# Kernel optimization log

Hardware: AMD Instinct MI355X
Metric: run time of the kernel (lower is better)

The kernel has to match this reference:

```python
import jax, jax.numpy as jnp
import numpy as np

B, T, Q, K, H = 8, 128, 64, 64, 4  # batch, agents, q_dim, kv_dim, heads; neighbors n = T-1


def setup_inputs() -> dict:
    key = jax.random.key(0)
    ks = jax.random.split(key, 9)
    s = 0.05
    return {
        "q_x": jax.random.normal(ks[0], (B, T, Q), dtype=jnp.float32),
        "kv_x": jax.random.normal(ks[1], (B, T, T - 1, K), dtype=jnp.float32),
        # nn.Linear weights stored (out_features, in_features), y = x @ W.T + b
        "Wk": jax.random.normal(ks[2], (H * K, K), dtype=jnp.float32) * s,      # tokeys (no bias)
        "Wq": jax.random.normal(ks[3], (H * K, Q), dtype=jnp.float32) * s,      # toqueries (no bias)
        "Wv": jax.random.normal(ks[4], (H * K, K + Q), dtype=jnp.float32) * s,  # tovalues
        "bv": jax.random.normal(ks[5], (H * K,), dtype=jnp.float32) * s,
        "bias": jax.random.uniform(ks[6], (K,), dtype=jnp.float32, minval=-0.1, maxval=0.1),
        "ws": jax.random.normal(ks[7], (K,), dtype=jnp.float32) * s,            # score_proj weight (1, K) -> (K,)
        "bs": jax.random.normal(ks[8], (), dtype=jnp.float32) * s,              # score_proj bias
    }


def reference(q_x, kv_x, Wk, Wq, Wv, bv, bias, ws, bs):
    b, t, n, k = kv_x.shape            # n = t - 1 neighbors
    q = q_x.shape[-1]
    h = Wk.shape[0] // k
    # key / query projections
    keys = jnp.einsum('btnk,ok->btno', kv_x, Wk).reshape(b, t, n, h, k)
    queries = jnp.einsum('btq,oq->bto', q_x, Wq).reshape(b, t, 1, h, k)
    # additive (Bahdanau) score: linear(tanh(keys + queries + bias)) -> scalar per (b,t,n,h)
    score = jnp.einsum('btnhk,k->btnh', jnp.tanh(keys + queries + bias), ws) + bs
    # values from concat(kv, broadcast query features)
    q_exp = jnp.broadcast_to(q_x[:, :, None, :], (b, t, n, q))
    value_input = jnp.concatenate([kv_x, q_exp], axis=-1)      # (b,t,n,k+q)
    values = (jnp.einsum('btnc,oc->btno', value_input, Wv) + bv).reshape(b, t, n, h, k)
    # softmax over neighbors, weighted sum of values
    w = jax.nn.softmax(score, axis=2)                          # (b,t,n,h)
    x = jnp.einsum('btnh,btnhk->bthk', w, values).reshape(b, t, h * k)
    return x
```

## Files before the change

### kernel.cpp

```cpp
#include <hip/hip_runtime.h>
#include <hip/hip_bf16.h>

#define NB 127
#define SCALE 2.885390081777927f

typedef __attribute__((ext_vector_type(8))) short bf16x8;
typedef __attribute__((ext_vector_type(4))) float f32x4;

#define WKP_S  0
#define WVP_S  16384
#define WQP_S  32768
#define WVQP_S 49152
#define WS_NEEDED ((size_t)(4 * 16384 * 2))

__device__ __forceinline__ short bfs(float f) {
  __hip_bfloat16 h = __float2bfloat16(f);
  return __builtin_bit_cast(short, h);
}
__device__ __forceinline__ unsigned packbf2(float a, float b) {
  unsigned lo = (unsigned short)bfs(a);
  unsigned hi = (unsigned short)bfs(b);
  return lo | (hi << 16);
}
__device__ __forceinline__ float b2f(short s) {
  unsigned u = ((unsigned)(unsigned short)s) << 16;
  return __builtin_bit_cast(float, u);
}
__device__ __forceinline__ bf16x8 gath_s(const float* __restrict__ p, float s) {
  float4 a = *(const float4*)p;
  float4 b = *(const float4*)(p + 4);
  bf16x8 f;
  f[0] = bfs(a.x * s); f[1] = bfs(a.y * s); f[2] = bfs(a.z * s); f[3] = bfs(a.w * s);
  f[4] = bfs(b.x * s); f[5] = bfs(b.y * s); f[6] = bfs(b.z * s); f[7] = bfs(b.w * s);
  return f;
}
__device__ __forceinline__ float sigt(float x) {
  return __builtin_amdgcn_rcpf(__builtin_amdgcn_exp2f(x) + 1.f);
}

__global__ __launch_bounds__(256, 2) void
pack_kernel(const float* __restrict__ Wk, const float* __restrict__ Wq,
            const float* __restrict__ Wv, short* __restrict__ dstall)
{
  const int blk = blockIdx.x;
  const int tid = threadIdx.x;
  const int m = blk >> 4, sub = blk & 15;
  const float* src; int stride, off, dsto; float scl;
  if (m == 0)      { src = Wk; stride = 64;  off = 0;  dsto = WKP_S;  scl = SCALE; }
  else if (m == 1) { src = Wv; stride = 128; off = 0;  dsto = WVP_S;  scl = 1.f; }
  else if (m == 2) { src = Wq; stride = 64;  off = 0;  dsto = WQP_S;  scl = SCALE; }
  else             { src = Wv; stride = 128; off = 64; dsto = WVQP_S; scl = 1.f; }
  short* dst = dstall + dsto;
  int i4 = sub * 256 + tid;
  int o = i4 >> 4, c4 = i4 & 15;
  float4 v = ((const float4*)(src + o * stride + off))[c4];
  int k0 = c4 * 4;
  int kt = k0 >> 5, gg = (k0 & 31) >> 3, j0 = k0 & 7;
  int head = o >> 6, nt = (o >> 4) & 3, ol = o & 15;
  int di = ((((head * 4 + nt) * 2 + kt) * 64) + gg * 16 + ol) * 8 + j0;
  *(uint2*)(dst + di) = make_uint2(packbf2(v.x * scl, v.y * scl),
                                   packbf2(v.z * scl, v.w * scl));
}

template <int PREP>
__global__ __launch_bounds__(256, 4) void
rnn_attn_kernel(const float* __restrict__ q_x, const float* __restrict__ kv_x,
                const float* __restrict__ Wk, const float* __restrict__ Wq,
                const float* __restrict__ Wv, const float* __restrict__ bv,
                const float* __restrict__ bias, const float* __restrict__ wsc,
                const short* __restrict__ pack, float* __restrict__ out)
{
  __shared__ __align__(16) unsigned char Atile[128 * 128];
  __shared__ float scs[4][128];
  __shared__ float4 qv_lds[4][4][4];

  const int tid = threadIdx.x;
  const int bt = blockIdx.x;
  const int lane = tid & 63;
  const int head = tid >> 6;
  const int l15 = lane & 15;
  const int g = lane >> 4;

  const float* kv = kv_x + (size_t)bt * (NB * 64);
  #pragma unroll
  for (int i = 0; i < 8; ++i) {
    int idx = i * 256 + tid;
    int row = idx >> 4, c = idx & 15;
    float4 v = (row < NB) ? ((const float4*)kv)[idx] : make_float4(0.f, 0.f, 0.f, 0.f);
    int byte = (row << 7) + (c << 3);
    byte ^= ((row & 7) << 4);
    *(uint2*)(&Atile[byte]) = make_uint2(packbf2(v.x, v.y), packbf2(v.z, v.w));
  }

  f32x4 qq[4];
  {
    bf16x8 qf0 = gath_s(q_x + bt * 64 + g * 8, 1.f);
    bf16x8 qf1 = gath_s(q_x + bt * 64 + 32 + g * 8, 1.f);
    #pragma unroll
    for (int nt = 0; nt < 4; ++nt) {
      bf16x8 wv0, wv1;
      if (PREP) {
        const bf16x8* pv = (const bf16x8*)(pack + WVQP_S);
        wv0 = pv[((head * 4 + nt) * 2 + 0) * 64 + lane];
        wv1 = pv[((head * 4 + nt) * 2 + 1) * 64 + lane];
      } else {
        int o = head * 64 + nt * 16 + l15;
        wv0 = gath_s(Wv + o * 128 + 64 + g * 8, 1.f);
        wv1 = gath_s(Wv + o * 128 + 64 + 32 + g * 8, 1.f);
      }
      float4 bv4 = ((const float4*)(bv + head * 64))[nt * 4 + g];
      f32x4 b = (f32x4){bv4.x, bv4.y, bv4.z, bv4.w};
      b = __builtin_amdgcn_mfma_f32_16x16x32_bf16(wv0, qf0, b, 0, 0, 0);
      b = __builtin_amdgcn_mfma_f32_16x16x32_bf16(wv1, qf1, b, 0, 0, 0);
      if (l15 == 0) qv_lds[head][nt][g] = make_float4(b[0], b[1], b[2], b[3]);
    }
    #pragma unroll
    for (int nt = 0; nt < 4; ++nt) {
      bf16x8 wq0, wq1;
      if (PREP) {
        const bf16x8* pw = (const bf16x8*)(pack + WQP_S);
        wq0 = pw[((head * 4 + nt) * 2 + 0) * 64 + lane];
        wq1 = pw[((head * 4 + nt) * 2 + 1) * 64 + lane];
      } else {
        int o = head * 64 + nt * 16 + l15;
        wq0 = gath_s(Wq + o * 64 + g * 8, SCALE);
        wq1 = gath_s(Wq + o * 64 + 32 + g * 8, SCALE);
      }
      float4 bs4 = ((const float4*)bias)[nt * 4 + g];
      f32x4 a = (f32x4){bs4.x * SCALE, bs4.y * SCALE, bs4.z * SCALE, bs4.w * SCALE};
      a = __builtin_amdgcn_mfma_f32_16x16x32_bf16(wq0, qf0, a, 0, 0, 0);
      a = __builtin_amdgcn_mfma_f32_16x16x32_bf16(wq1, qf1, a, 0, 0, 0);
      qq[nt] = a;
    }
  }

  __syncthreads();

  #pragma unroll
  for (int h = 0; h < 2; ++h) {
    bf16x8 b00, b01, b10, b11;
    if (PREP) {
      const bf16x8* pw = (const bf16x8*)(pack + WKP_S);
      b00 = pw[((head * 4 + 2 * h + 0) * 2 + 0) * 64 + lane];
      b01 = pw[((head * 4 + 2 * h + 0) * 2 + 1) * 64 + lane];
      b10 = pw[((head * 4 + 2 * h + 1) * 2 + 0) * 64 + lane];
      b11 = pw[((head * 4 + 2 * h + 1) * 2 + 1) * 64 + lane];
    } else {
      int o0 = head * 64 + (2 * h) * 16 + l15;
      b00 = gath_s(Wk + o0 * 64 + g * 8, SCALE);
      b01 = gath_s(Wk + o0 * 64 + 32 + g * 8, SCALE);
      b10 = gath_s(Wk + (o0 + 16) * 64 + g * 8, SCALE);
      b11 = gath_s(Wk + (o0 + 16) * 64 + 32 + g * 8, SCALE);
    }
    float4 ta = ((const float4*)wsc)[(2 * h) * 4 + g];
    float4 tb = ((const float4*)wsc)[(2 * h + 1) * 4 + g];
    f32x4 wsa = (f32x4){-2.f * ta.x, -2.f * ta.y, -2.f * ta.z, -2.f * ta.w};
    f32x4 wsb = (f32x4){-2.f * tb.x, -2.f * tb.y, -2.f * tb.z, -2.f * tb.w};
    f32x4 qa = qq[2 * h], qb = qq[2 * h + 1];

    #pragma unroll 1
    for (int mt = 0; mt < 8; ++mt) {
      int row = mt * 16 + l15;
      int byte0 = (row << 7) + g * 16;
      int swz = (l15 & 7) << 4;
      bf16x8 a0 = *(const bf16x8*)(&Atile[byte0 ^ swz]);
      bf16x8 a1 = *(const bf16x8*)(&Atile[(byte0 + 64) ^ swz]);
      f32x4 acc = qa;
      acc = __builtin_amdgcn_mfma_f32_16x16x32_bf16(b00, a0, acc, 0, 0, 0);
      acc = __builtin_amdgcn_mfma_f32_16x16x32_bf16(b01, a1, acc, 0, 0, 0);
      f32x4 acc2 = qb;
      acc2 = __builtin_amdgcn_mfma_f32_16x16x32_bf16(b10, a0, acc2, 0, 0, 0);
      acc2 = __builtin_amdgcn_mfma_f32_16x16x32_bf16(b11, a1, acc2, 0, 0, 0);
      float p0 = wsa[0] * sigt(acc[0]);
      float p1 = wsa[1] * sigt(acc[1]);
      float p2 = wsa[2] * sigt(acc[2]);
      float p3 = wsa[3] * sigt(acc[3]);
      p0 = fmaf(wsb[0], sigt(acc2[0]), p0);
      p1 = fmaf(wsb[1], sigt(acc2[1]), p1);
      p2 = fmaf(wsb[2], sigt(acc2[2]), p2);
      p3 = fmaf(wsb[3], sigt(acc2[3]), p3);
      float p = (p0 + p1) + (p2 + p3);
      p += __shfl_xor(p, 16);
      p += __shfl_xor(p, 32);
      if (g == 0) {
        int idx = mt * 16 + l15;
        scs[head][idx] = h ? (scs[head][idx] + p) : p;
      }
    }
  }

  {
    float s0 = scs[head][l15 + 0],  s1 = scs[head][l15 + 16];
    float s2 = scs[head][l15 + 32], s3 = scs[head][l15 + 48];
    float s4 = scs[head][l15 + 64], s5 = scs[head][l15 + 80];
    float s6 = scs[head][l15 + 96], s7 = scs[head][l15 + 112];
    if (l15 == 15) s7 = -3.0e38f;
    float m = fmaxf(fmaxf(fmaxf(s0, s1), fmaxf(s2, s3)),
                    fmaxf(fmaxf(s4, s5), fmaxf(s6, s7)));
    #pragma unroll
    for (int d = 1; d < 16; d <<= 1) m = fmaxf(m, __shfl_xor(m, d));
    float e0 = __expf(s0 - m), e1 = __expf(s1 - m), e2 = __expf(s2 - m), e3 = __expf(s3 - m);
    float e4 = __expf(s4 - m), e5 = __expf(s5 - m), e6 = __expf(s6 - m), e7 = __expf(s7 - m);
    float sum = ((e0 + e1) + (e2 + e3)) + ((e4 + e5) + (e6 + e7));
    #pragma unroll
    for (int d = 1; d < 16; d <<= 1) sum += __shfl_xor(sum, d);
    float inv = __builtin_amdgcn_rcpf(sum);
    if (g == 0) {
      scs[head][l15 + 0]  = e0 * inv; scs[head][l15 + 16] = e1 * inv;
      scs[head][l15 + 32] = e2 * inv; scs[head][l15 + 48] = e3 * inv;
      scs[head][l15 + 64] = e4 * inv; scs[head][l15 + 80] = e5 * inv;
      scs[head][l15 + 96] = e6 * inv; scs[head][l15 + 112] = e7 * inv;
    }
  }

  float pvp0[8], pvp1[8];
  #pragma unroll
  for (int j = 0; j < 8; ++j) { pvp0[j] = 0.f; pvp1[j] = 0.f; }
  #pragma unroll 1
  for (int mt = 0; mt < 8; ++mt) {
    int row = mt * 16 + l15;
    int byte0 = (row << 7) + g * 16;
    int swz = (l15 & 7) << 4;
    bf16x8 a0 = *(const bf16x8*)(&Atile[byte0 ^ swz]);
    bf16x8 a1 = *(const bf16x8*)(&Atile[(byte0 + 64) ^ swz]);
    float w = scs[head][mt * 16 + l15];
    #pragma unroll
    for (int j = 0; j < 8; ++j) {
      pvp0[j] = fmaf(w, b2f(a0[j]), pvp0[j]);
      pvp1[j] = fmaf(w, b2f(a1[j]), pvp1[j]);
    }
  }
  bf16x8 pa0, pa1;
  #pragma unroll
  for (int j = 0; j < 8; ++j) { pa0[j] = bfs(pvp0[j]); pa1[j] = bfs(pvp1[j]); }

  float tt[4];
  #pragma unroll 2
  for (int nt = 0; nt < 4; ++nt) {
    bf16x8 bw0, bw1;
    if (PREP) {
      const bf16x8* pw = (const bf16x8*)(pack + WVP_S);
      bw0 = pw[((head * 4 + nt) * 2 + 0) * 64 + lane];
      bw1 = pw[((head * 4 + nt) * 2 + 1) * 64 + lane];
    } else {
      int o = head * 64 + nt * 16 + l15;
      bw0 = gath_s(Wv + o * 128 + g * 8, 1.f);
      bw1 = gath_s(Wv + o * 128 + 32 + g * 8, 1.f);
    }
    f32x4 c = (f32x4){0.f, 0.f, 0.f, 0.f};
    c = __builtin_amdgcn_mfma_f32_16x16x32_bf16(pa0, bw0, c, 0, 0, 0);
    c = __builtin_amdgcn_mfma_f32_16x16x32_bf16(pa1, bw1, c, 0, 0, 0);
    float t = (c[0] + c[1]) + (c[2] + c[3]);
    t += __shfl_xor(t, 16);
    t += __shfl_xor(t, 32);
    tt[nt] = t;
  }

  float v = tt[0];
  v = (g == 1) ? tt[1] : v;
  v = (g == 2) ? tt[2] : v;
  v = (g == 3) ? tt[3] : v;
  float qv = ((const float*)&qv_lds[head][g][l15 >> 2])[l15 & 3];
  out[bt * 256 + head * 64 + lane] = v + qv;
}

extern "C" void kernel_launch(void* const* d_in, const int* in_sizes, int n_in,
                              void* d_out, int out_size, void* d_ws, size_t ws_size,
                              hipStream_t stream) {
  const float* q_x  = (const float*)d_in[0];
  const float* kv_x = (const float*)d_in[1];
  const float* Wk   = (const float*)d_in[2];
  const float* Wq   = (const float*)d_in[3];
  const float* Wv   = (const float*)d_in[4];
  const float* bv   = (const float*)d_in[5];
  const float* bias = (const float*)d_in[6];
  const float* wsc  = (const float*)d_in[7];
  float* out = (float*)d_out;
  short* pack = (short*)d_ws;

  if (ws_size >= WS_NEEDED) {
    pack_kernel<<<64, 256, 0, stream>>>(Wk, Wq, Wv, pack);
    rnn_attn_kernel<1><<<1024, 256, 0, stream>>>(q_x, kv_x, Wk, Wq, Wv, bv, bias, wsc, pack, out);
  } else {
    rnn_attn_kernel<0><<<1024, 256, 0, stream>>>(q_x, kv_x, Wk, Wq, Wv, bv, bias, wsc, pack, out);
  }
}
```

Baseline: 29.58 us.

## Fuse score, unnormalized softmax and weighted sum into one pass over neighbors

```diff
diff --git a/kernel.cpp b/kernel.cpp
--- a/kernel.cpp
+++ b/kernel.cpp
@@ -63,7 +63,7 @@
 }
 
 template <int PREP>
-__global__ __launch_bounds__(256, 4) void
+__global__ __launch_bounds__(256, 2) void
 rnn_attn_kernel(const float* __restrict__ q_x, const float* __restrict__ kv_x,
                 const float* __restrict__ Wk, const float* __restrict__ Wq,
                 const float* __restrict__ Wv, const float* __restrict__ bv,
@@ -71,7 +71,6 @@
                 const short* __restrict__ pack, float* __restrict__ out)
 {
   __shared__ __align__(16) unsigned char Atile[128 * 128];
-  __shared__ float scs[4][128];
   __shared__ float4 qv_lds[4][4][4];
 
   const int tid = threadIdx.x;
@@ -134,86 +133,26 @@
     }
   }
 
-  __syncthreads();
-
-  #pragma unroll
-  for (int h = 0; h < 2; ++h) {
-    bf16x8 b00, b01, b10, b11;
+  f32x4 ws4[4];
+  bf16x8 bk[4][2];
+  #pragma unroll
+  for (int nt = 0; nt < 4; ++nt) {
+    float4 t = ((const float4*)wsc)[nt * 4 + g];
+    ws4[nt] = (f32x4){-2.f * t.x, -2.f * t.y, -2.f * t.z, -2.f * t.w};
     if (PREP) {
       const bf16x8* pw = (const bf16x8*)(pack + WKP_S);
-      b00 = pw[((head * 4 + 2 * h + 0) * 2 + 0) * 64 + lane];
-      b01 = pw[((head * 4 + 2 * h + 0) * 2 + 1) * 64 + lane];
-      b10 = pw[((head * 4 + 2 * h + 1) * 2 + 0) * 64 + lane];
-      b11 = pw[((head * 4 + 2 * h + 1) * 2 + 1) * 64 + lane];
+      bk[nt][0] = pw[((head * 4 + nt) * 2 + 0) * 64 + lane];
+      bk[nt][1] = pw[((head * 4 + nt) * 2 + 1) * 64 + lane];
     } else {
-      int o0 = head * 64 + (2 * h) * 16 + l15;
-      b00 = gath_s(Wk + o0 * 64 + g * 8, SCALE);
-      b01 = gath_s(Wk + o0 * 64 + 32 + g * 8, SCALE);
-      b10 = gath_s(Wk + (o0 + 16) * 64 + g * 8, SCALE);
-      b11 = gath_s(Wk + (o0 + 16) * 64 + 32 + g * 8, SCALE);
-    }
-    float4 ta = ((const float4*)wsc)[(2 * h) * 4 + g];
-    float4 tb = ((const float4*)wsc)[(2 * h + 1) * 4 + g];
-    f32x4 wsa = (f32x4){-2.f * ta.x, -2.f * ta.y, -2.f * ta.z, -2.f * ta.w};
-    f32x4 wsb = (f32x4){-2.f * tb.x, -2.f * tb.y, -2.f * tb.z, -2.f * tb.w};
-    f32x4 qa = qq[2 * h], qb = qq[2 * h + 1];
-
-    #pragma unroll 1
-    for (int mt = 0; mt < 8; ++mt) {
-      int row = mt * 16 + l15;
-      int byte0 = (row << 7) + g * 16;
-      int swz = (l15 & 7) << 4;
-      bf16x8 a0 = *(const bf16x8*)(&Atile[byte0 ^ swz]);
-      bf16x8 a1 = *(const bf16x8*)(&Atile[(byte0 + 64) ^ swz]);
-      f32x4 acc = qa;
-      acc = __builtin_amdgcn_mfma_f32_16x16x32_bf16(b00, a0, acc, 0, 0, 0);
-      acc = __builtin_amdgcn_mfma_f32_16x16x32_bf16(b01, a1, acc, 0, 0, 0);
-      f32x4 acc2 = qb;
-      acc2 = __builtin_amdgcn_mfma_f32_16x16x32_bf16(b10, a0, acc2, 0, 0, 0);
-      acc2 = __builtin_amdgcn_mfma_f32_16x16x32_bf16(b11, a1, acc2, 0, 0, 0);
-      float p0 = wsa[0] * sigt(acc[0]);
-      float p1 = wsa[1] * sigt(acc[1]);
-      float p2 = wsa[2] * sigt(acc[2]);
-      float p3 = wsa[3] * sigt(acc[3]);
-      p0 = fmaf(wsb[0], sigt(acc2[0]), p0);
-      p1 = fmaf(wsb[1], sigt(acc2[1]), p1);
-      p2 = fmaf(wsb[2], sigt(acc2[2]), p2);
-      p3 = fmaf(wsb[3], sigt(acc2[3]), p3);
-      float p = (p0 + p1) + (p2 + p3);
-      p += __shfl_xor(p, 16);
-      p += __shfl_xor(p, 32);
-      if (g == 0) {
-        int idx = mt * 16 + l15;
-        scs[head][idx] = h ? (scs[head][idx] + p) : p;
-      }
-    }
-  }
-
-  {
-    float s0 = scs[head][l15 + 0],  s1 = scs[head][l15 + 16];
-    float s2 = scs[head][l15 + 32], s3 = scs[head][l15 + 48];
-    float s4 = scs[head][l15 + 64], s5 = scs[head][l15 + 80];
-    float s6 = scs[head][l15 + 96], s7 = scs[head][l15 + 112];
-    if (l15 == 15) s7 = -3.0e38f;
-    float m = fmaxf(fmaxf(fmaxf(s0, s1), fmaxf(s2, s3)),
-                    fmaxf(fmaxf(s4, s5), fmaxf(s6, s7)));
-    #pragma unroll
-    for (int d = 1; d < 16; d <<= 1) m = fmaxf(m, __shfl_xor(m, d));
-    float e0 = __expf(s0 - m), e1 = __expf(s1 - m), e2 = __expf(s2 - m), e3 = __expf(s3 - m);
-    float e4 = __expf(s4 - m), e5 = __expf(s5 - m), e6 = __expf(s6 - m), e7 = __expf(s7 - m);
-    float sum = ((e0 + e1) + (e2 + e3)) + ((e4 + e5) + (e6 + e7));
-    #pragma unroll
-    for (int d = 1; d < 16; d <<= 1) sum += __shfl_xor(sum, d);
-    float inv = __builtin_amdgcn_rcpf(sum);
-    if (g == 0) {
-      scs[head][l15 + 0]  = e0 * inv; scs[head][l15 + 16] = e1 * inv;
-      scs[head][l15 + 32] = e2 * inv; scs[head][l15 + 48] = e3 * inv;
-      scs[head][l15 + 64] = e4 * inv; scs[head][l15 + 80] = e5 * inv;
-      scs[head][l15 + 96] = e6 * inv; scs[head][l15 + 112] = e7 * inv;
-    }
-  }
-
-  float pvp0[8], pvp1[8];
+      int o = head * 64 + nt * 16 + l15;
+      bk[nt][0] = gath_s(Wk + o * 64 + g * 8, SCALE);
+      bk[nt][1] = gath_s(Wk + o * 64 + 32 + g * 8, SCALE);
+    }
+  }
+
+  __syncthreads();
+
+  float pvp0[8], pvp1[8], z = 0.f;
   #pragma unroll
   for (int j = 0; j < 8; ++j) { pvp0[j] = 0.f; pvp1[j] = 0.f; }
   #pragma unroll 1
@@ -223,16 +162,65 @@
     int swz = (l15 & 7) << 4;
     bf16x8 a0 = *(const bf16x8*)(&Atile[byte0 ^ swz]);
     bf16x8 a1 = *(const bf16x8*)(&Atile[(byte0 + 64) ^ swz]);
-    float w = scs[head][mt * 16 + l15];
+    float pp0, pp1, pp2, pp3;
+    {
+      f32x4 acc = qq[0];
+      acc = __builtin_amdgcn_mfma_f32_16x16x32_bf16(bk[0][0], a0, acc, 0, 0, 0);
+      acc = __builtin_amdgcn_mfma_f32_16x16x32_bf16(bk[0][1], a1, acc, 0, 0, 0);
+      pp0 = ws4[0][0] * sigt(acc[0]);
+      pp0 = fmaf(ws4[0][1], sigt(acc[1]), pp0);
+      pp0 = fmaf(ws4[0][2], sigt(acc[2]), pp0);
+      pp0 = fmaf(ws4[0][3], sigt(acc[3]), pp0);
+    }
+    {
+      f32x4 acc = qq[1];
+      acc = __builtin_amdgcn_mfma_f32_16x16x32_bf16(bk[1][0], a0, acc, 0, 0, 0);
+      acc = __builtin_amdgcn_mfma_f32_16x16x32_bf16(bk[1][1], a1, acc, 0, 0, 0);
+      pp1 = ws4[1][0] * sigt(acc[0]);
+      pp1 = fmaf(ws4[1][1], sigt(acc[1]), pp1);
+      pp1 = fmaf(ws4[1][2], sigt(acc[2]), pp1);
+      pp1 = fmaf(ws4[1][3], sigt(acc[3]), pp1);
+    }
+    {
+      f32x4 acc = qq[2];
+      acc = __builtin_amdgcn_mfma_f32_16x16x32_bf16(bk[2][0], a0, acc, 0, 0, 0);
+      acc = __builtin_amdgcn_mfma_f32_16x16x32_bf16(bk[2][1], a1, acc, 0, 0, 0);
+      pp2 = ws4[2][0] * sigt(acc[0]);
+      pp2 = fmaf(ws4[2][1], sigt(acc[1]), pp2);
+      pp2 = fmaf(ws4[2][2], sigt(acc[2]), pp2);
+      pp2 = fmaf(ws4[2][3], sigt(acc[3]), pp2);
+    }
+    {
+      f32x4 acc = qq[3];
+      acc = __builtin_amdgcn_mfma_f32_16x16x32_bf16(bk[3][0], a0, acc, 0, 0, 0);
+      acc = __builtin_amdgcn_mfma_f32_16x16x32_bf16(bk[3][1], a1, acc, 0, 0, 0);
+      pp3 = ws4[3][0] * sigt(acc[0]);
+      pp3 = fmaf(ws4[3][1], sigt(acc[1]), pp3);
+      pp3 = fmaf(ws4[3][2], sigt(acc[2]), pp3);
+      pp3 = fmaf(ws4[3][3], sigt(acc[3]), pp3);
+    }
+    float p = (pp0 + pp1) + (pp2 + pp3);
+    p += __shfl_xor(p, 16);
+    p += __shfl_xor(p, 32);
+    float e = __expf(p);
+    if (mt == 7 && l15 == 15) e = 0.f;
+    z += e;
     #pragma unroll
     for (int j = 0; j < 8; ++j) {
-      pvp0[j] = fmaf(w, b2f(a0[j]), pvp0[j]);
-      pvp1[j] = fmaf(w, b2f(a1[j]), pvp1[j]);
-    }
-  }
+      pvp0[j] = fmaf(e, b2f(a0[j]), pvp0[j]);
+      pvp1[j] = fmaf(e, b2f(a1[j]), pvp1[j]);
+    }
+  }
+
+  z += __shfl_xor(z, 1);
+  z += __shfl_xor(z, 2);
+  z += __shfl_xor(z, 4);
+  z += __shfl_xor(z, 8);
+  float rz = __builtin_amdgcn_rcpf(z);
+
   bf16x8 pa0, pa1;
   #pragma unroll
-  for (int j = 0; j < 8; ++j) { pa0[j] = bfs(pvp0[j]); pa1[j] = bfs(pvp1[j]); }
+  for (int j = 0; j < 8; ++j) { pa0[j] = bfs(pvp0[j] * rz); pa1[j] = bfs(pvp1[j] * rz); }
 
   float tt[4];
   #pragma unroll 2
```

Measured after the change: 28.00 us. -5.3%, faster.
